# Optimization experiments

Measured on AMD Instinct MI355X. Metric: run time of the kernel, lower is better.

## Reference

```python
import jax, jax.numpy as jnp
import numpy as np

DIM, HEADS, K = 64, 4, 7
HEAD_DIM = DIM // HEADS
SCALE = HEAD_DIM ** -0.5  # qk_scale = head_dim ** -0.5


def setup_inputs() -> dict:
    key = jax.random.key(0)
    ks = jax.random.split(key, 6)
    B, H, W, SH, SW = 1, 192, 192, 12, 12
    x = jax.random.normal(ks[0], (B, DIM, H, W), dtype=jnp.float32)
    # soft pixel->superpixel association probabilities in [0,1)
    sims = jax.random.uniform(ks[1], (B, H, W, SH, SW), dtype=jnp.float32)
    s = DIM ** -0.5
    w_q = jax.random.normal(ks[2], (DIM, DIM), dtype=jnp.float32) * s
    w_k = jax.random.normal(ks[3], (DIM, DIM), dtype=jnp.float32) * s
    w_v = jax.random.normal(ks[4], (DIM, DIM), dtype=jnp.float32) * s
    w_proj = jax.random.normal(ks[5], (DIM, DIM), dtype=jnp.float32) * s
    return {"x": x, "sims": sims, "w_q": w_q, "w_k": w_k, "w_v": w_v, "w_proj": w_proj}


def _forward(x, sims, w_q, w_k, w_v, w_proj):
    B, C, H, W = x.shape
    SH, SW = sims.shape[-2:]
    h, d = HEADS, C // HEADS
    xf = jnp.transpose(x, (0, 2, 3, 1))                 # [B,H,W,C]
    q = (xf @ w_q).reshape(B, H, W, h, d)
    k = (xf @ w_k).reshape(B, H, W, h, d)
    v = (xf @ w_v).reshape(B, H, W, h, d)
    # NATTEN-style clamped neighborhood window starts
    sy = jnp.clip(jnp.arange(H) - K // 2, 0, H - K)     # [H]
    sx = jnp.clip(jnp.arange(W) - K // 2, 0, W - K)     # [W]
    # get_indices: nearest-interp of superpixel label grid -> hard cell per pixel
    si = (jnp.arange(H) * SH) // H                      # [H]
    sj = (jnp.arange(W) * SW) // W                      # [W]
    logits, masks = [], []
    for ky in range(K):                                  # fixed small kernel loop
        ny = sy + ky
        for kx in range(K):
            nx = sx + kx
            k_n = k[:, ny][:, :, nx]                    # [B,H,W,h,d] gathered neighbor keys
            logits.append(jnp.einsum('byxhd,byxhd->bhyx', q, k_n))
            # prob. neighbor pixel j belongs to query pixel i's superpixel cell
            masks.append(sims[:, ny[:, None], nx[None, :], si[:, None], sj[None, :]])  # [B,H,W]
    logits = jnp.stack(logits, -1)                      # [B,h,H,W,K*K]
    mask = jnp.stack(masks, -1)[:, None]                # [B,1,H,W,K*K]
    attn = jax.nn.softmax(SCALE * logits * mask, axis=-1)
    attn_m = attn * mask                                # soft-mask weighted aggregation
    out = jnp.zeros((B, h, H, W, d), x.dtype)
    o = 0
    for ky in range(K):
        ny = sy + ky
        for kx in range(K):
            nx = sx + kx
            v_n = jnp.transpose(v[:, ny][:, :, nx], (0, 3, 1, 2, 4))  # [B,h,H,W,d]
            out = out + attn_m[..., o, None] * v_n
            o += 1
    out = jnp.transpose(out, (0, 2, 3, 1, 4)).reshape(B, H, W, C)
    out = out @ w_proj
    return jnp.transpose(out, (0, 3, 1, 2))             # back to NCHW


def reference(x, sims, w_q, w_k, w_v, w_proj):
    return _forward(x, sims, w_q, w_k, w_v, w_proj)
```

## Files before the change

### kernel.cpp

```cpp
#include <hip/hip_runtime.h>
#include <math.h>

#define HH 192
#define WW 192
#define NPIX (HH * WW)
#define SCALE 0.25f
#define C1 0.36067376f

#define HR 10
#define HC 14
#define NSLOT 160
#define VOFF 160

typedef __attribute__((ext_vector_type(8))) _Float16 f16x8;
typedef __attribute__((ext_vector_type(4))) _Float16 f16x4;
typedef __attribute__((ext_vector_type(4))) float f32x4;

#if __has_builtin(__builtin_amdgcn_exp2f)
#define EXP2(x) __builtin_amdgcn_exp2f(x)
#else
#define EXP2(x) exp2f(x)
#endif

#define MFMA16(a, b, c) __builtin_amdgcn_mfma_f32_16x16x16f16((a), (b), (c), 0, 0, 0)

static __device__ __forceinline__ short f16s(float f)
{
    _Float16 h = (_Float16)f;
    short s; __builtin_memcpy(&s, &h, 2); return s;
}

static __device__ __forceinline__ unsigned int pack_f16(float a, float b)
{
    unsigned short ul = (unsigned short)f16s(a);
    unsigned short uh = (unsigned short)f16s(b);
    return ((unsigned int)uh << 16) | ul;
}

__global__ __launch_bounds__(256) void qkv_mfma(
    const float* __restrict__ x,
    const float* __restrict__ wq, const float* __restrict__ wk,
    const float* __restrict__ wv, const float* __restrict__ wp,
    unsigned int* __restrict__ qg, unsigned int* __restrict__ kg,
    unsigned int* __restrict__ vg, short* __restrict__ wT)
{
    const int t = threadIdx.x;

    if (blockIdx.x == NPIX / 64) {
        #pragma unroll
        for (int i = 0; i < 16; ++i) {
            const int idx = i * 256 + t;
            const int n = idx >> 6, k = idx & 63;
            wT[(192 + n) * 64 + k] = f16s(wp[k * 64 + n]);
        }
        return;
    }

    __shared__ short lds[(64 + 192) * 72];
    short* xT = lds;
    short* wTs = lds + 64 * 72;
    const int px0 = blockIdx.x * 64;

    #pragma unroll
    for (int r = 0; r < 16; ++r) {
        const int idx = r * 256 + t;
        const int cin = idx >> 6, pxl = idx & 63;
        xT[pxl * 72 + cin] = f16s(x[(size_t)cin * NPIX + px0 + pxl]);
    }
    #pragma unroll
    for (int m = 0; m < 3; ++m) {
        const float* ws = (m == 0) ? wq : (m == 1) ? wk : wv;
        #pragma unroll
        for (int r = 0; r < 16; ++r) {
            const int idx = r * 256 + t;
            const int k = idx >> 6, n = idx & 63;
            wTs[(m * 64 + n) * 72 + k] = f16s(ws[k * 64 + n]);
        }
    }
    __syncthreads();

    const int lane = t & 63;
    const int wid  = t >> 6;
    const int l15  = lane & 15;
    const int kg4  = lane >> 4;

    f32x4 acc[12];
    #pragma unroll
    for (int nt = 0; nt < 12; ++nt) acc[nt] = (f32x4){0.f, 0.f, 0.f, 0.f};

    #pragma unroll
    for (int ks = 0; ks < 2; ++ks) {
        const f16x8 a = *reinterpret_cast<const f16x8*>(
            &xT[(wid * 16 + l15) * 72 + ks * 32 + kg4 * 8]);
        #pragma unroll
        for (int nt = 0; nt < 12; ++nt) {
            const f16x8 b = *reinterpret_cast<const f16x8*>(
                &wTs[(nt * 16 + l15) * 72 + ks * 32 + kg4 * 8]);
            acc[nt] = __builtin_amdgcn_mfma_f32_16x16x32_f16(a, b, acc[nt], 0, 0, 0);
        }
    }

    #pragma unroll
    for (int nt = 0; nt < 12; ++nt) {
        unsigned int* dst = (nt < 4) ? qg : (nt < 8) ? kg : vg;
        const int dwb = (nt & 3) * 8 + (l15 >> 1);
        #pragma unroll
        for (int r = 0; r < 4; ++r) {
            const float val = acc[nt][r];
            const float par = __shfl_xor(val, 1, 64);
            if (!(lane & 1)) {
                const int opx = px0 + wid * 16 + kg4 * 4 + r;
                dst[(size_t)opx * 32 + dwb] = pack_f16(val, par);
            }
        }
    }
}

__global__ __launch_bounds__(512) void attn_proj(
    const unsigned int* __restrict__ qg,
    const unsigned int* __restrict__ kg,
    const unsigned int* __restrict__ vg,
    const float* __restrict__ sims,
    const short* __restrict__ wT,
    float* __restrict__ out)
{
    __shared__ unsigned int smem[VOFF + 4 * 160 * 8];

    const int bid = blockIdx.x;
    const int tl = (bid & 7) * 144 + (bid >> 3);
    const int ty = tl / 24, tx = tl - ty * 24;
    const int Y0 = ty * 4, X0 = tx * 8;
    int hy0 = Y0 - 3; hy0 = hy0 < 0 ? 0 : (hy0 > HH - HR ? HH - HR : hy0);
    int hx0 = X0 - 3; hx0 = hx0 < 0 ? 0 : (hx0 > WW - HC ? WW - HC : hx0);
    const int t = threadIdx.x;

    #pragma unroll
    for (int i = 0; i < 3; ++i) {
        const int idx = i * 512 + t;
        if (idx < 1280) {
            const int n = idx >> 3, u = idx & 7;
            const int ry = n >> 4, cx = n & 15;
            uint4 vv = make_uint4(0u, 0u, 0u, 0u);
            if (cx < HC) {
                const int np = (hy0 + ry) * WW + hx0 + cx;
                vv = *reinterpret_cast<const uint4*>(vg + (size_t)np * 32 + u * 4);
            }
            const int h = u >> 1, hf = u & 1;
            *reinterpret_cast<uint4*>(smem + VOFF + h * 1280 + n * 8 + hf * 4) = vv;
        }
    }
    if (t < NSLOT) {
        const int ry = t >> 4, cx = t & 15;
        float m = 0.f;
        if (cx < HC) {
            const int np = (hy0 + ry) * WW + hx0 + cx;
            const int sbase = (Y0 >> 4) * 12 + (X0 >> 4);
            m = sims[np * 144 + sbase];
        }
        reinterpret_cast<float*>(smem)[t] = m * C1;
    }
    __syncthreads();

    const int w    = t >> 6;
    const int h    = w & 3;
    const int qt   = w >> 2;
    const int lane = t & 63;
    const int l15  = lane & 15;
    const int kg4  = lane >> 4;
    const float* mC = reinterpret_cast<const float*>(smem);

    const unsigned vbyte = (unsigned)(uintptr_t)smem + VOFF * 4
                         + h * 5120 + lane * 8;
    f16x4 vf[10];
#define TRREAD(I, IMM) \
    asm volatile("ds_read_b64_tr_b16 %0, %1 offset:" IMM \
                 : "=v"(vf[I]) : "v"(vbyte))
    TRREAD(0, "0");    TRREAD(1, "512");  TRREAD(2, "1024"); TRREAD(3, "1536");
    TRREAD(4, "2048"); TRREAD(5, "2560"); TRREAD(6, "3072"); TRREAD(7, "3584");
    TRREAD(8, "4096"); TRREAD(9, "4608");
#undef TRREAD

    const unsigned int* kgp = kg + (size_t)(hy0 * WW + hx0 + l15) * 32
                            + h * 8 + kg4 * 2;
    f16x4 kf[10];
    #pragma unroll
    for (int nt = 0; nt < 10; ++nt)
        kf[nt] = *reinterpret_cast<const f16x4*>(kgp + (size_t)nt * (WW * 32));

    const int q = qt * 16 + l15;
    const int qry = q >> 3, qcx = q & 7;
    const int y = Y0 + qry, x = X0 + qcx;
    int sy = y - 3; sy = sy < 0 ? 0 : (sy > HH - 7 ? HH - 7 : sy);
    int sx = x - 3; sx = sx < 0 ? 0 : (sx > WW - 7 ? WW - 7 : sx);
    const int wy = sy - hy0, wx = sx - hx0;

    const f16x4 qb = *reinterpret_cast<const f16x4*>(
        qg + (size_t)(y * WW + x) * 32 + h * 8 + kg4 * 2);

    float vx[4];
    #pragma unroll
    for (int rr = 0; rr < 4; ++rr)
        vx[rr] = ((unsigned)(kg4 * 4 + rr - wx) < 7u) ? 1.f : 0.f;

    float Ss = 0.f;
    f16x4 pt[10];
    #pragma unroll
    for (int nt = 0; nt < 10; ++nt) {
        const f32x4 s = MFMA16(kf[nt], qb, ((f32x4){0.f, 0.f, 0.f, 0.f}));
        const f32x4 mcv = *reinterpret_cast<const f32x4*>(mC + nt * 16 + kg4 * 4);
        const float vy = ((unsigned)(nt - wy) < 7u) ? 1.f : 0.f;
        float pf[4];
        #pragma unroll
        for (int e = 0; e < 4; ++e) {
            const float u = s[e] * mcv[e];
            const float p = EXP2(u);
            const float pv = p * vy * vx[e];
            Ss += pv;
            pf[e] = pv * mcv[e];
        }
        pt[nt] = (f16x4){(_Float16)pf[0], (_Float16)pf[1],
                         (_Float16)pf[2], (_Float16)pf[3]};
    }
    Ss += __shfl_xor(Ss, 16, 64);
    Ss += __shfl_xor(Ss, 32, 64);
    const float invq = 1.f / (C1 * Ss);

    asm volatile("s_waitcnt lgkmcnt(0)" ::: "memory");
    __builtin_amdgcn_sched_barrier(0);
    f32x4 o = (f32x4){0.f, 0.f, 0.f, 0.f};
    #pragma unroll
    for (int nt = 0; nt < 10; ++nt)
        o = MFMA16(vf[nt], pt[nt], o);

    __syncthreads();
    {
        short* A = reinterpret_cast<short*>(smem);
        const f16x4 ov = (f16x4){
            (_Float16)(o[0] * invq), (_Float16)(o[1] * invq),
            (_Float16)(o[2] * invq), (_Float16)(o[3] * invq)};
        *reinterpret_cast<f16x4*>(&A[q * 72 + h * 16 + kg4 * 4]) = ov;
    }
    __syncthreads();

    const short* A_lds = reinterpret_cast<const short*>(smem);
    const int mt  = w & 1;
    const int nt4 = w >> 1;

    f16x8 afrag[2];
    #pragma unroll
    for (int ks = 0; ks < 2; ++ks)
        afrag[ks] = *reinterpret_cast<const f16x8*>(
            &A_lds[(mt * 16 + l15) * 72 + ks * 32 + kg4 * 8]);

    {
        const int n = nt4 * 16 + l15;
        f32x4 pacc = (f32x4){0.f, 0.f, 0.f, 0.f};
        #pragma unroll
        for (int ks = 0; ks < 2; ++ks) {
            const f16x8 b = *reinterpret_cast<const f16x8*>(
                &wT[(192 + n) * 64 + ks * 32 + kg4 * 8]);
            pacc = __builtin_amdgcn_mfma_f32_16x16x32_f16(afrag[ks], b, pacc, 0, 0, 0);
        }
        const int pr = mt * 16 + kg4 * 4;
        const int gy = Y0 + (pr >> 3), gx = X0 + (pr & 7);
        *reinterpret_cast<float4*>(out + (size_t)n * NPIX + gy * WW + gx) =
            make_float4(pacc[0], pacc[1], pacc[2], pacc[3]);
    }
}

extern "C" void kernel_launch(void* const* d_in, const int* in_sizes, int n_in,
                              void* d_out, int out_size, void* d_ws, size_t ws_size,
                              hipStream_t stream)
{
    const float* x    = (const float*)d_in[0];
    const float* sims = (const float*)d_in[1];
    const float* wq   = (const float*)d_in[2];
    const float* wk   = (const float*)d_in[3];
    const float* wv   = (const float*)d_in[4];
    const float* wp   = (const float*)d_in[5];
    float* out = (float*)d_out;

    unsigned int* qg = (unsigned int*)d_ws;
    unsigned int* kg = qg + (size_t)NPIX * 32;
    unsigned int* vg = kg + (size_t)NPIX * 32;
    short* wT = (short*)(vg + (size_t)NPIX * 32);

    qkv_mfma<<<NPIX / 64 + 1, 256, 0, stream>>>(x, wq, wk, wv, wp, qg, kg, vg, wT);
    attn_proj<<<1152, 512, 0, stream>>>(qg, kg, vg, sims, wT, out);
}
```

Baseline: 43.66 us.

## Halve attention block to four waves, each looping over two query tiles

The attention kernel now runs 256 threads per block instead of 512. Each wave handles one head and loops over both 16-query tiles, reusing the K and V fragments it already loaded in registers. The PV MFMA is fused into the softmax loop so the probability tile does not need to be held across the whole loop. The output tile gets its own LDS region, which removes one barrier. The projection loop now covers two N tiles per wave. This cuts redundant K/V fragment loads and block overhead, but each wave does twice the sequential work and there are fewer waves available to hide latency.

```diff
diff --git a/kernel.cpp b/kernel.cpp
--- a/kernel.cpp
+++ b/kernel.cpp
@@ -11,6 +11,7 @@
 #define HC 14
 #define NSLOT 160
 #define VOFF 160
+#define AOFF 5280
 
 typedef __attribute__((ext_vector_type(8))) _Float16 f16x8;
 typedef __attribute__((ext_vector_type(4))) _Float16 f16x4;
@@ -116,7 +117,7 @@
     }
 }
 
-__global__ __launch_bounds__(512) void attn_proj(
+__global__ __launch_bounds__(256) void attn_proj(
     const unsigned int* __restrict__ qg,
     const unsigned int* __restrict__ kg,
     const unsigned int* __restrict__ vg,
@@ -124,7 +125,7 @@
     const short* __restrict__ wT,
     float* __restrict__ out)
 {
-    __shared__ unsigned int smem[VOFF + 4 * 160 * 8];
+    __shared__ unsigned int smem[AOFF + 1152];
 
     const int bid = blockIdx.x;
     const int tl = (bid & 7) * 144 + (bid >> 3);
@@ -135,19 +136,17 @@
     const int t = threadIdx.x;
 
     #pragma unroll
-    for (int i = 0; i < 3; ++i) {
-        const int idx = i * 512 + t;
-        if (idx < 1280) {
-            const int n = idx >> 3, u = idx & 7;
-            const int ry = n >> 4, cx = n & 15;
-            uint4 vv = make_uint4(0u, 0u, 0u, 0u);
-            if (cx < HC) {
-                const int np = (hy0 + ry) * WW + hx0 + cx;
-                vv = *reinterpret_cast<const uint4*>(vg + (size_t)np * 32 + u * 4);
-            }
-            const int h = u >> 1, hf = u & 1;
-            *reinterpret_cast<uint4*>(smem + VOFF + h * 1280 + n * 8 + hf * 4) = vv;
-        }
+    for (int i = 0; i < 5; ++i) {
+        const int idx = i * 256 + t;
+        const int n = idx >> 3, u = idx & 7;
+        const int ry = n >> 4, cx = n & 15;
+        uint4 vv = make_uint4(0u, 0u, 0u, 0u);
+        if (cx < HC) {
+            const int np = (hy0 + ry) * WW + hx0 + cx;
+            vv = *reinterpret_cast<const uint4*>(vg + (size_t)np * 32 + u * 4);
+        }
+        const int h = u >> 1, hf = u & 1;
+        *reinterpret_cast<uint4*>(smem + VOFF + h * 1280 + n * 8 + hf * 4) = vv;
     }
     if (t < NSLOT) {
         const int ry = t >> 4, cx = t & 15;
@@ -161,9 +160,7 @@
     }
     __syncthreads();
 
-    const int w    = t >> 6;
-    const int h    = w & 3;
-    const int qt   = w >> 2;
+    const int h    = t >> 6;
     const int lane = t & 63;
     const int l15  = lane & 15;
     const int kg4  = lane >> 4;
@@ -187,54 +184,53 @@
     for (int nt = 0; nt < 10; ++nt)
         kf[nt] = *reinterpret_cast<const f16x4*>(kgp + (size_t)nt * (WW * 32));
 
-    const int q = qt * 16 + l15;
-    const int qry = q >> 3, qcx = q & 7;
-    const int y = Y0 + qry, x = X0 + qcx;
-    int sy = y - 3; sy = sy < 0 ? 0 : (sy > HH - 7 ? HH - 7 : sy);
-    int sx = x - 3; sx = sx < 0 ? 0 : (sx > WW - 7 ? WW - 7 : sx);
-    const int wy = sy - hy0, wx = sx - hx0;
-
-    const f16x4 qb = *reinterpret_cast<const f16x4*>(
-        qg + (size_t)(y * WW + x) * 32 + h * 8 + kg4 * 2);
-
-    float vx[4];
-    #pragma unroll
-    for (int rr = 0; rr < 4; ++rr)
-        vx[rr] = ((unsigned)(kg4 * 4 + rr - wx) < 7u) ? 1.f : 0.f;
-
-    float Ss = 0.f;
-    f16x4 pt[10];
-    #pragma unroll
-    for (int nt = 0; nt < 10; ++nt) {
-        const f32x4 s = MFMA16(kf[nt], qb, ((f32x4){0.f, 0.f, 0.f, 0.f}));
-        const f32x4 mcv = *reinterpret_cast<const f32x4*>(mC + nt * 16 + kg4 * 4);
-        const float vy = ((unsigned)(nt - wy) < 7u) ? 1.f : 0.f;
-        float pf[4];
-        #pragma unroll
-        for (int e = 0; e < 4; ++e) {
-            const float u = s[e] * mcv[e];
-            const float p = EXP2(u);
-            const float pv = p * vy * vx[e];
-            Ss += pv;
-            pf[e] = pv * mcv[e];
-        }
-        pt[nt] = (f16x4){(_Float16)pf[0], (_Float16)pf[1],
-                         (_Float16)pf[2], (_Float16)pf[3]};
-    }
-    Ss += __shfl_xor(Ss, 16, 64);
-    Ss += __shfl_xor(Ss, 32, 64);
-    const float invq = 1.f / (C1 * Ss);
-
     asm volatile("s_waitcnt lgkmcnt(0)" ::: "memory");
     __builtin_amdgcn_sched_barrier(0);
-    f32x4 o = (f32x4){0.f, 0.f, 0.f, 0.f};
-    #pragma unroll
-    for (int nt = 0; nt < 10; ++nt)
-        o = MFMA16(vf[nt], pt[nt], o);
-
-    __syncthreads();
-    {
-        short* A = reinterpret_cast<short*>(smem);
+
+    short* A = reinterpret_cast<short*>(smem + AOFF);
+
+    #pragma unroll 1
+    for (int qt = 0; qt < 2; ++qt) {
+        const int q = qt * 16 + l15;
+        const int qry = q >> 3, qcx = q & 7;
+        const int y = Y0 + qry, x = X0 + qcx;
+        int sy = y - 3; sy = sy < 0 ? 0 : (sy > HH - 7 ? HH - 7 : sy);
+        int sx = x - 3; sx = sx < 0 ? 0 : (sx > WW - 7 ? WW - 7 : sx);
+        const int wy = sy - hy0, wx = sx - hx0;
+
+        const f16x4 qb = *reinterpret_cast<const f16x4*>(
+            qg + (size_t)(y * WW + x) * 32 + h * 8 + kg4 * 2);
+
+        float vx[4];
+        #pragma unroll
+        for (int rr = 0; rr < 4; ++rr)
+            vx[rr] = ((unsigned)(kg4 * 4 + rr - wx) < 7u) ? 1.f : 0.f;
+
+        float Ss = 0.f;
+        f32x4 o = (f32x4){0.f, 0.f, 0.f, 0.f};
+        #pragma unroll
+        for (int nt = 0; nt < 10; ++nt) {
+            const f32x4 s = MFMA16(kf[nt], qb, ((f32x4){0.f, 0.f, 0.f, 0.f}));
+            const f32x4 mcv = *reinterpret_cast<const f32x4*>(
+                mC + nt * 16 + kg4 * 4);
+            const float vy = ((unsigned)(nt - wy) < 7u) ? 1.f : 0.f;
+            float pf[4];
+            #pragma unroll
+            for (int e = 0; e < 4; ++e) {
+                const float u = s[e] * mcv[e];
+                const float p = EXP2(u);
+                const float pv = p * vy * vx[e];
+                Ss += pv;
+                pf[e] = pv * mcv[e];
+            }
+            const f16x4 pt = (f16x4){(_Float16)pf[0], (_Float16)pf[1],
+                                     (_Float16)pf[2], (_Float16)pf[3]};
+            o = MFMA16(vf[nt], pt, o);
+        }
+        Ss += __shfl_xor(Ss, 16, 64);
+        Ss += __shfl_xor(Ss, 32, 64);
+        const float invq = 1.f / (C1 * Ss);
+
         const f16x4 ov = (f16x4){
             (_Float16)(o[0] * invq), (_Float16)(o[1] * invq),
             (_Float16)(o[2] * invq), (_Float16)(o[3] * invq)};
@@ -242,9 +238,9 @@
     }
     __syncthreads();
 
-    const short* A_lds = reinterpret_cast<const short*>(smem);
-    const int mt  = w & 1;
-    const int nt4 = w >> 1;
+    const short* A_lds = reinterpret_cast<const short*>(smem + AOFF);
+    const int mt  = h & 1;
+    const int np2 = h >> 1;
 
     f16x8 afrag[2];
     #pragma unroll
@@ -252,8 +248,9 @@
         afrag[ks] = *reinterpret_cast<const f16x8*>(
             &A_lds[(mt * 16 + l15) * 72 + ks * 32 + kg4 * 8]);
 
-    {
-        const int n = nt4 * 16 + l15;
+    #pragma unroll
+    for (int nt2 = 0; nt2 < 2; ++nt2) {
+        const int n = (np2 * 2 + nt2) * 16 + l15;
         f32x4 pacc = (f32x4){0.f, 0.f, 0.f, 0.f};
         #pragma unroll
         for (int ks = 0; ks < 2; ++ks) {
@@ -286,5 +283,5 @@
     short* wT = (short*)(vg + (size_t)NPIX * 32);
 
     qkv_mfma<<<NPIX / 64 + 1, 256, 0, stream>>>(x, wq, wk, wv, wp, qg, kg, vg, wT);
-    attn_proj<<<1152, 512, 0, stream>>>(qg, kg, vg, sims, wT, out);
-}
+    attn_proj<<<1152, 256, 0, stream>>>(qg, kg, vg, sims, wT, out);
+}
```

Result: faster. 36.54 us (-16.3%).
